# Kernel tuning notes

Hardware: AMD Instinct MI355X
Metric: run time of the kernel (lower is better)

The kernel has to match this reference:

```python
import jax, jax.numpy as jnp
import numpy as np
import math

B, C, N, M = 4, 128, 4096, 4096

def setup_inputs() -> dict:
    key = jax.random.key(0)
    ks = jax.random.split(key, 8)
    return {
        "x1": jax.random.normal(ks[0], (B, C, N), dtype=jnp.float32),
        "p1": jax.random.normal(ks[1], (B, 3, N), dtype=jnp.float32),
        "x2": jax.random.normal(ks[2], (B, C, M), dtype=jnp.float32),
        "p2": jax.random.normal(ks[3], (B, 3, M), dtype=jnp.float32),
        "Wq": jax.random.normal(ks[4], (C, C), dtype=jnp.float32) * 0.05,
        "Wk": jax.random.normal(ks[5], (C, C), dtype=jnp.float32) * 0.05,
        "Wv": jax.random.normal(ks[6], (C, C), dtype=jnp.float32) * 0.05,
        "Wpos": jax.random.normal(ks[7], (C, 3), dtype=jnp.float32) * 0.05,
    }

def reference(x1, p1, x2, p2, Wq, Wk, Wv, Wpos):
    # Conv1d with kernel_size=1, no bias == per-point matmul over channel dim.
    # NOTE: original forward uses self.pos for BOTH p1 and p2 (pos1 conv unused).
    pos = jnp.einsum('ck,bkn->bcn', Wpos, p1)   # [B,C,N]
    pos1 = jnp.einsum('ck,bkm->bcm', Wpos, p2)  # [B,C,M]
    q = jnp.einsum('dc,bcn->bdn', Wq, x1 + pos)   # [B,C,N]
    k = jnp.einsum('dc,bcm->bdm', Wk, x2 + pos1)  # [B,C,M]
    v = jnp.einsum('dc,bcm->bdm', Wv, x2)         # [B,C,M]
    scale = math.sqrt(q.shape[1])  # sqrt(C) -- q.shape[-2] in (B,C,N) layout
    energy = jnp.einsum('bcn,bcm->bnm', q, k) / scale  # [B,N,M]
    attention = jax.nn.softmax(energy, axis=-1)
    vout = jnp.einsum('bnm,bcm->bnc', attention, v)    # [B,N,C]
    out = jnp.swapaxes(vout, 1, 2) + x1                # [B,C,N] residual
    return jnp.swapaxes(out, 1, 2)                     # [B,N,C]
```

## Files before the change

### kernel.cpp

```cpp
#include <hip/hip_runtime.h>
#include <hip/hip_bf16.h>

#define B_ 4
#define C_ 128
#define N_ 4096
#define M_ 4096

typedef __bf16 bf16;
typedef __bf16 bf16x8 __attribute__((ext_vector_type(8)));
typedef float f32x4 __attribute__((ext_vector_type(4)));
typedef float f32x16 __attribute__((ext_vector_type(16)));

#define MFMA16(a, b, c) __builtin_amdgcn_mfma_f32_16x16x32_bf16(a, b, c, 0, 0, 0)
#define MFMA32(a, b, c) __builtin_amdgcn_mfma_f32_32x32x16_bf16(a, b, c, 0, 0, 0)

__device__ inline bf16x8 cvt8(const float* p8) {
    float4 a = *(const float4*)p8;
    float4 b = *(const float4*)(p8 + 4);
    bf16x8 r;
    r[0] = (bf16)a.x; r[1] = (bf16)a.y; r[2] = (bf16)a.z; r[3] = (bf16)a.w;
    r[4] = (bf16)b.x; r[5] = (bf16)b.y; r[6] = (bf16)b.z; r[7] = (bf16)b.w;
    return r;
}

__device__ inline void gll16(const bf16* g, bf16* l) {
    __builtin_amdgcn_global_load_lds(
        (const __attribute__((address_space(1))) void*)g,
        (__attribute__((address_space(3))) void*)l, 16, 0, 0);
}

__global__ __launch_bounds__(768) void proj_kernel(
    const float* __restrict__ x1, const float* __restrict__ p1,
    const float* __restrict__ x2, const float* __restrict__ p2,
    const float* __restrict__ Wq, const float* __restrict__ Wk,
    const float* __restrict__ Wv, const float* __restrict__ Wpos,
    bf16* __restrict__ Qt, bf16* __restrict__ Kt, bf16* __restrict__ Vt) {
    __shared__ __align__(16) bf16 xp1[64 * 136];
    __shared__ __align__(16) bf16 xp2[64 * 136];
    __shared__ __align__(16) bf16 xr2[64 * 136];
    __shared__ float pp1[3 * 64], pp2[3 * 64], wls[384];

    const int t = threadIdx.x;
    const int b = blockIdx.y;
    const int n0 = blockIdx.x * 64;

    if (t < 48) {
        int k3 = t / 16, i4 = (t & 15) * 4;
        *(float4*)&pp1[k3 * 64 + i4] = *(const float4*)(p1 + ((size_t)b * 3 + k3) * N_ + n0 + i4);
    } else if (t < 96) {
        int tt = t - 48;
        int k3 = tt / 16, i4 = (tt & 15) * 4;
        *(float4*)&pp2[k3 * 64 + i4] = *(const float4*)(p2 + ((size_t)b * 3 + k3) * N_ + n0 + i4);
    } else if (t < 192) {
        int i4 = (t - 96) * 4;
        *(float4*)&wls[i4] = *(const float4*)(Wpos + i4);
    }
    __syncthreads();

    for (int s = t; s < 2048; s += 768) {
        int c = s >> 4, n4 = (s & 15) * 4;
        float4 xv = *(const float4*)(x1 + ((size_t)b * C_ + c) * N_ + n0 + n4);
        float w0 = wls[c * 3 + 0], w1 = wls[c * 3 + 1], w2 = wls[c * 3 + 2];
        const float* xa = &xv.x;
        #pragma unroll
        for (int j = 0; j < 4; ++j) {
            float pos = w0 * pp1[n4 + j] + w1 * pp1[64 + n4 + j] + w2 * pp1[128 + n4 + j];
            xp1[(n4 + j) * 136 + c] = (bf16)(xa[j] + pos);
        }
    }
    for (int s = t; s < 2048; s += 768) {
        int c = s >> 4, n4 = (s & 15) * 4;
        float4 xv = *(const float4*)(x2 + ((size_t)b * C_ + c) * N_ + n0 + n4);
        float w0 = wls[c * 3 + 0], w1 = wls[c * 3 + 1], w2 = wls[c * 3 + 2];
        const float* xa = &xv.x;
        #pragma unroll
        for (int j = 0; j < 4; ++j) {
            float pos = w0 * pp2[n4 + j] + w1 * pp2[64 + n4 + j] + w2 * pp2[128 + n4 + j];
            xp2[(n4 + j) * 136 + c] = (bf16)(xa[j] + pos);
            xr2[(n4 + j) * 136 + c] = (bf16)xa[j];
        }
    }
    __syncthreads();

    const int w = t >> 6;
    const int lane = t & 63;
    const int col = lane & 15, quad = lane >> 4;
    const int role = w >> 2, band = w & 3;
    const int nl = band * 16 + col;
    const int n = n0 + nl;

    const bf16* src = (role == 0) ? xp1 : (role == 1) ? xp2 : xr2;
    const float* Wm = (role == 0) ? Wq : (role == 1) ? Wk : Wv;

    bf16x8 bx[4];
    #pragma unroll
    for (int cs = 0; cs < 4; ++cs)
        bx[cs] = *(const bf16x8*)&src[nl * 136 + cs * 32 + quad * 8];

    #pragma unroll
    for (int dt = 0; dt < 8; ++dt) {
        f32x4 acc = {0.f, 0.f, 0.f, 0.f};
        #pragma unroll
        for (int cs = 0; cs < 4; ++cs) {
            bf16x8 wf = cvt8(Wm + (dt * 16 + col) * 128 + cs * 32 + quad * 8);
            acc = MFMA16(wf, bx[cs], acc);
        }
        if (role < 2) {
            bf16* Ot = (role == 0) ? Qt : Kt;
            union { ushort4 u4; bf16 h[4]; } pk;
            #pragma unroll
            for (int r = 0; r < 4; ++r) pk.h[r] = (bf16)acc[r];
            *(ushort4*)(Ot + ((size_t)b * N_ + n) * C_ + dt * 16 + quad * 4) = pk.u4;
        } else {
            #pragma unroll
            for (int r = 0; r < 4; ++r)
                Vt[((size_t)b * C_ + dt * 16 + quad * 4 + r) * (size_t)M_ + n] = (bf16)acc[r];
        }
    }
}

__global__ __launch_bounds__(256, 2) void attn_kernel(
    const bf16* __restrict__ Qt, const bf16* __restrict__ Kt,
    const bf16* __restrict__ Vt, const float* __restrict__ x1,
    float* __restrict__ out) {
    __shared__ __align__(16) char smem[75776];
    bf16* kb = (bf16*)smem;
    bf16* vb = (bf16*)(smem + 32768);
    bf16* pb = (bf16*)(smem + 65536);

    const int t = threadIdx.x;
    const int w = t >> 6;
    const int lane = t & 63;
    const int col = lane & 31;
    const int hi = lane >> 5;

    const int g0 = blockIdx.x;
    const int xcd = g0 & 7;
    const int b = xcd >> 1;
    const int qt = (xcd & 1) + ((g0 >> 3) << 1);
    const int n0 = qt * 32;

    const float KS = 0.12752107168406815f;

    const bf16* Kbase = Kt + (size_t)b * M_ * C_;
    const bf16* Vbase = Vt + (size_t)b * C_ * M_;

    bf16x8 qf[8];
    {
        const bf16* Qb = Qt + ((size_t)b * N_ + n0 + col) * C_ + hi * 8;
        #pragma unroll
        for (int cs = 0; cs < 8; ++cs)
            qf[cs] = *(const bf16x8*)(Qb + cs * 16);
    }

    f32x16 oacc[4];
    #pragma unroll
    for (int i = 0; i < 4; ++i)
        #pragma unroll
        for (int j = 0; j < 16; ++j) oacc[i][j] = 0.f;
    float lacc[16];
    #pragma unroll
    for (int r = 0; r < 16; ++r) lacc[r] = 0.f;

    const int key_l = (w << 5) + col;
    const char* kbp = (const char*)kb + key_l * 256;
    const int kxor = (key_l & 7) << 4;
    bf16* pbw = pb + w * 1280;

    auto stageK = [&](int m0) {
        #pragma unroll
        for (int i = 0; i < 8; ++i) {
            int g = ((w << 3) + i) * 64 + lane;
            int key = g >> 4;
            int sp = (g & 15) ^ (key & 7);
            gll16(Kbase + (size_t)(m0 + key) * C_ + sp * 8, kb + ((w << 3) + i) * 512);
        }
    };
    auto stageV = [&](int m0) {
        #pragma unroll
        for (int i = 0; i < 8; ++i) {
            int g = ((w << 3) + i) * 64 + lane;
            int c = g >> 4;
            int sp = (g & 15) ^ (c & 7);
            gll16(Vbase + (size_t)c * M_ + m0 + sp * 8, vb + ((w << 3) + i) * 512);
        }
    };

    stageK(0);
    stageV(0);
    __syncthreads();

    for (int ch = 0; ch < 32; ++ch) {
        f32x16 sacc;
        #pragma unroll
        for (int j = 0; j < 16; ++j) sacc[j] = 0.f;
        __builtin_amdgcn_s_setprio(1);
        #pragma unroll
        for (int cs = 0; cs < 8; ++cs) {
            bf16x8 kf = *(const bf16x8*)(kbp + ((((cs << 1) + hi) << 4) ^ kxor));
            sacc = MFMA32(qf[cs], kf, sacc);
        }
        __builtin_amdgcn_s_setprio(0);

        __syncthreads();
        if (ch < 31) stageK((ch + 1) << 7);

        #pragma unroll
        for (int r = 0; r < 16; ++r) {
            float e = fminf(sacc[r] * KS, 60.f);
            float p = __builtin_amdgcn_exp2f(e);
            lacc[r] += p;
            int q = (r & 3) + ((r >> 2) << 3) + (hi << 2);
            pbw[q * 40 + col] = (bf16)p;
        }
        asm volatile("s_waitcnt lgkmcnt(0)" ::: "memory");

        bf16x8 af0 = *(const bf16x8*)&pbw[col * 40 + hi * 8];
        bf16x8 af1 = *(const bf16x8*)&pbw[col * 40 + 16 + hi * 8];

        __builtin_amdgcn_s_setprio(1);
        #pragma unroll
        for (int ct = 0; ct < 4; ++ct) {
            int c = (ct << 5) + col;
            const char* vbp = (const char*)vb + c * 256;
            int vxor = (c & 7) << 4;
            bf16x8 vf0 = *(const bf16x8*)(vbp + ((((w << 2) + hi) << 4) ^ vxor));
            bf16x8 vf1 = *(const bf16x8*)(vbp + ((((w << 2) + 2 + hi) << 4) ^ vxor));
            oacc[ct] = MFMA32(af0, vf0, oacc[ct]);
            oacc[ct] = MFMA32(af1, vf1, oacc[ct]);
        }
        __builtin_amdgcn_s_setprio(0);

        __syncthreads();
        if (ch < 31) stageV((ch + 1) << 7);
    }

    __syncthreads();

    float* obuf = (float*)smem;
    float* lps  = (float*)(smem + 67584);

    #pragma unroll
    for (int r = 0; r < 16; ++r)
        #pragma unroll
        for (int off = 1; off < 32; off <<= 1)
            lacc[r] += __shfl_xor(lacc[r], off, 64);

    if (col == 0) {
        #pragma unroll
        for (int r = 0; r < 16; ++r) {
            int q = (r & 3) + ((r >> 2) << 3) + (hi << 2);
            lps[(w << 5) + q] = lacc[r];
        }
    }
    #pragma unroll
    for (int ct = 0; ct < 4; ++ct)
        #pragma unroll
        for (int r = 0; r < 16; ++r) {
            int q = (r & 3) + ((r >> 2) << 3) + (hi << 2);
            obuf[w * 4224 + q * 132 + (ct << 5) + col] = oacc[ct][r];
        }
    __syncthreads();

    const int c2 = lane << 1;
    #pragma unroll
    for (int j = 0; j < 8; ++j) {
        int q = (w << 3) + j;
        float s0 = 0.f, s1 = 0.f;
        #pragma unroll
        for (int p = 0; p < 4; ++p) {
            s0 += obuf[p * 4224 + q * 132 + c2];
            s1 += obuf[p * 4224 + q * 132 + c2 + 1];
        }
        float lsum = lps[q] + lps[32 + q] + lps[64 + q] + lps[96 + q];
        float linv = 1.0f / lsum;
        int n = n0 + q;
        float o0 = s0 * linv + x1[((size_t)b * C_ + c2) * N_ + n];
        float o1 = s1 * linv + x1[((size_t)b * C_ + c2 + 1) * N_ + n];
        *(float2*)&out[((size_t)b * N_ + n) * C_ + c2] = make_float2(o0, o1);
    }
}

extern "C" void kernel_launch(void* const* d_in, const int* in_sizes, int n_in,
                              void* d_out, int out_size, void* d_ws, size_t ws_size,
                              hipStream_t stream) {
    const float* x1   = (const float*)d_in[0];
    const float* p1   = (const float*)d_in[1];
    const float* x2   = (const float*)d_in[2];
    const float* p2   = (const float*)d_in[3];
    const float* Wq   = (const float*)d_in[4];
    const float* Wk   = (const float*)d_in[5];
    const float* Wv   = (const float*)d_in[6];
    const float* Wpos = (const float*)d_in[7];
    float* out = (float*)d_out;

    bf16* Qt = (bf16*)d_ws;
    bf16* Kt = Qt + (size_t)B_ * N_ * C_;
    bf16* Vt = Kt + (size_t)B_ * M_ * C_;

    proj_kernel<<<dim3(64, B_), dim3(768), 0, stream>>>(
        x1, p1, x2, p2, Wq, Wk, Wv, Wpos, Qt, Kt, Vt);
    attn_kernel<<<dim3(512), dim3(256), 0, stream>>>(Qt, Kt, Vt, x1, out);
}
```

Measured before the change: 169.1 us.

## Transpose S MFMA to keep P in registers and loosen attention barriers

The attention kernel now computes S^T (K as the A operand) and splits it across two accumulators. It builds the P operand in registers with packed bf16 conversion and a cross-half lane shuffle, which removes the LDS round trip for P and the per-row shuffle reductions. The __syncthreads calls become vmcnt-based waits plus raw s_barrier so the next K/V tile loads overlap compute, and the LDS swizzle is widened to 16. The weights are also pre-converted to bf16 by a new small kernel that writes into the output buffer as scratch. This trades an extra launch and more fragile hand-written synchronization for less LDS traffic and fewer stalls.

```diff
diff --git a/kernel.cpp b/kernel.cpp
--- a/kernel.cpp
+++ b/kernel.cpp
@@ -14,26 +14,35 @@
 #define MFMA16(a, b, c) __builtin_amdgcn_mfma_f32_16x16x32_bf16(a, b, c, 0, 0, 0)
 #define MFMA32(a, b, c) __builtin_amdgcn_mfma_f32_32x32x16_bf16(a, b, c, 0, 0, 0)
 
-__device__ inline bf16x8 cvt8(const float* p8) {
-    float4 a = *(const float4*)p8;
-    float4 b = *(const float4*)(p8 + 4);
-    bf16x8 r;
-    r[0] = (bf16)a.x; r[1] = (bf16)a.y; r[2] = (bf16)a.z; r[3] = (bf16)a.w;
-    r[4] = (bf16)b.x; r[5] = (bf16)b.y; r[6] = (bf16)b.z; r[7] = (bf16)b.w;
-    return r;
-}
-
 __device__ inline void gll16(const bf16* g, bf16* l) {
     __builtin_amdgcn_global_load_lds(
         (const __attribute__((address_space(1))) void*)g,
         (__attribute__((address_space(3))) void*)l, 16, 0, 0);
 }
 
+__device__ inline unsigned cvtpk(float a, float b) {
+    unsigned r;
+    asm("v_cvt_pk_bf16_f32 %0, %1, %2" : "=v"(r) : "v"(a), "v"(b));
+    return r;
+}
+
+__global__ __launch_bounds__(256) void wcvt_kernel(
+    const float* __restrict__ Wq, const float* __restrict__ Wk,
+    const float* __restrict__ Wv, bf16* __restrict__ Wb) {
+    int i = (blockIdx.x * 256 + threadIdx.x) * 4;
+    const float* src = (i < 16384) ? Wq : (i < 32768) ? Wk : Wv;
+    int off = i & 16383;
+    float4 v = *(const float4*)(src + off);
+    union { ushort4 u4; bf16 h[4]; } pk;
+    pk.h[0] = (bf16)v.x; pk.h[1] = (bf16)v.y;
+    pk.h[2] = (bf16)v.z; pk.h[3] = (bf16)v.w;
+    *(ushort4*)(Wb + i) = pk.u4;
+}
+
 __global__ __launch_bounds__(768) void proj_kernel(
     const float* __restrict__ x1, const float* __restrict__ p1,
     const float* __restrict__ x2, const float* __restrict__ p2,
-    const float* __restrict__ Wq, const float* __restrict__ Wk,
-    const float* __restrict__ Wv, const float* __restrict__ Wpos,
+    const bf16* __restrict__ Wb, const float* __restrict__ Wpos,
     bf16* __restrict__ Qt, bf16* __restrict__ Kt, bf16* __restrict__ Vt) {
     __shared__ __align__(16) bf16 xp1[64 * 136];
     __shared__ __align__(16) bf16 xp2[64 * 136];
@@ -90,7 +99,7 @@
     const int n = n0 + nl;
 
     const bf16* src = (role == 0) ? xp1 : (role == 1) ? xp2 : xr2;
-    const float* Wm = (role == 0) ? Wq : (role == 1) ? Wk : Wv;
+    const bf16* Wm = Wb + role * 16384;
 
     bf16x8 bx[4];
     #pragma unroll
@@ -102,7 +111,7 @@
         f32x4 acc = {0.f, 0.f, 0.f, 0.f};
         #pragma unroll
         for (int cs = 0; cs < 4; ++cs) {
-            bf16x8 wf = cvt8(Wm + (dt * 16 + col) * 128 + cs * 32 + quad * 8);
+            bf16x8 wf = *(const bf16x8*)(Wm + (dt * 16 + col) * 128 + cs * 32 + quad * 8);
             acc = MFMA16(wf, bx[cs], acc);
         }
         if (role < 2) {
@@ -123,10 +132,9 @@
     const bf16* __restrict__ Qt, const bf16* __restrict__ Kt,
     const bf16* __restrict__ Vt, const float* __restrict__ x1,
     float* __restrict__ out) {
-    __shared__ __align__(16) char smem[75776];
+    __shared__ __align__(16) char smem[66048];
     bf16* kb = (bf16*)smem;
     bf16* vb = (bf16*)(smem + 32768);
-    bf16* pb = (bf16*)(smem + 65536);
 
     const int t = threadIdx.x;
     const int w = t >> 6;
@@ -158,21 +166,18 @@
     for (int i = 0; i < 4; ++i)
         #pragma unroll
         for (int j = 0; j < 16; ++j) oacc[i][j] = 0.f;
-    float lacc[16];
-    #pragma unroll
-    for (int r = 0; r < 16; ++r) lacc[r] = 0.f;
+    float lacc = 0.f;
 
     const int key_l = (w << 5) + col;
     const char* kbp = (const char*)kb + key_l * 256;
-    const int kxor = (key_l & 7) << 4;
-    bf16* pbw = pb + w * 1280;
+    const int kxor = (key_l & 15) << 4;
 
     auto stageK = [&](int m0) {
         #pragma unroll
         for (int i = 0; i < 8; ++i) {
             int g = ((w << 3) + i) * 64 + lane;
             int key = g >> 4;
-            int sp = (g & 15) ^ (key & 7);
+            int sp = (g & 15) ^ (key & 15);
             gll16(Kbase + (size_t)(m0 + key) * C_ + sp * 8, kb + ((w << 3) + i) * 512);
         }
     };
@@ -181,49 +186,80 @@
         for (int i = 0; i < 8; ++i) {
             int g = ((w << 3) + i) * 64 + lane;
             int c = g >> 4;
-            int sp = (g & 15) ^ (c & 7);
+            int sp = (g & 15) ^ (c & 15);
             gll16(Vbase + (size_t)c * M_ + m0 + sp * 8, vb + ((w << 3) + i) * 512);
         }
     };
 
     stageK(0);
     stageV(0);
-    __syncthreads();
 
     for (int ch = 0; ch < 32; ++ch) {
-        f32x16 sacc;
-        #pragma unroll
-        for (int j = 0; j < 16; ++j) sacc[j] = 0.f;
+        asm volatile("s_waitcnt vmcnt(8)" ::: "memory");
+        __builtin_amdgcn_sched_barrier(0);
+
+        f32x16 s0a, s1a;
+        #pragma unroll
+        for (int j = 0; j < 16; ++j) { s0a[j] = 0.f; s1a[j] = 0.f; }
         __builtin_amdgcn_s_setprio(1);
         #pragma unroll
-        for (int cs = 0; cs < 8; ++cs) {
+        for (int cs = 0; cs < 4; ++cs) {
             bf16x8 kf = *(const bf16x8*)(kbp + ((((cs << 1) + hi) << 4) ^ kxor));
-            sacc = MFMA32(qf[cs], kf, sacc);
+            s0a = MFMA32(kf, qf[cs], s0a);
+        }
+        #pragma unroll
+        for (int cs = 4; cs < 8; ++cs) {
+            bf16x8 kf = *(const bf16x8*)(kbp + ((((cs << 1) + hi) << 4) ^ kxor));
+            s1a = MFMA32(kf, qf[cs], s1a);
         }
         __builtin_amdgcn_s_setprio(0);
 
-        __syncthreads();
-        if (ch < 31) stageK((ch + 1) << 7);
-
+        if (ch < 31) {
+            asm volatile("s_waitcnt lgkmcnt(0)" ::: "memory");
+            __builtin_amdgcn_sched_barrier(0);
+            stageK((ch + 1) << 7);
+        }
+
+        float p[16];
         #pragma unroll
         for (int r = 0; r < 16; ++r) {
-            float e = fminf(sacc[r] * KS, 60.f);
-            float p = __builtin_amdgcn_exp2f(e);
-            lacc[r] += p;
-            int q = (r & 3) + ((r >> 2) << 3) + (hi << 2);
-            pbw[q * 40 + col] = (bf16)p;
-        }
-        asm volatile("s_waitcnt lgkmcnt(0)" ::: "memory");
-
-        bf16x8 af0 = *(const bf16x8*)&pbw[col * 40 + hi * 8];
-        bf16x8 af1 = *(const bf16x8*)&pbw[col * 40 + 16 + hi * 8];
+            float e = fminf((s0a[r] + s1a[r]) * KS, 60.f);
+            p[r] = __builtin_amdgcn_exp2f(e);
+        }
+        {
+            float s01 = (p[0] + p[1]) + (p[2] + p[3]);
+            float s23 = (p[4] + p[5]) + (p[6] + p[7]);
+            float s45 = (p[8] + p[9]) + (p[10] + p[11]);
+            float s67 = (p[12] + p[13]) + (p[14] + p[15]);
+            lacc += (s01 + s23) + (s45 + s67);
+        }
+        unsigned W0 = cvtpk(p[0], p[1]),  W1 = cvtpk(p[2], p[3]);
+        unsigned W2 = cvtpk(p[4], p[5]),  W3 = cvtpk(p[6], p[7]);
+        unsigned W4 = cvtpk(p[8], p[9]),  W5 = cvtpk(p[10], p[11]);
+        unsigned W6 = cvtpk(p[12], p[13]), W7 = cvtpk(p[14], p[15]);
+        unsigned X0 = hi ? W0 : W2, X1 = hi ? W1 : W3;
+        unsigned Y0 = hi ? W4 : W6, Y1 = hi ? W5 : W7;
+        X0 = __shfl_xor(X0, 32, 64);  X1 = __shfl_xor(X1, 32, 64);
+        Y0 = __shfl_xor(Y0, 32, 64);  Y1 = __shfl_xor(Y1, 32, 64);
+        uint4 u0, u1;
+        u0.x = hi ? X0 : W0;  u0.y = hi ? X1 : W1;
+        u0.z = hi ? W2 : X0;  u0.w = hi ? W3 : X1;
+        u1.x = hi ? Y0 : W4;  u1.y = hi ? Y1 : W5;
+        u1.z = hi ? W6 : Y0;  u1.w = hi ? W7 : Y1;
+        bf16x8 af0 = __builtin_bit_cast(bf16x8, u0);
+        bf16x8 af1 = __builtin_bit_cast(bf16x8, u1);
+
+        if (ch < 31) asm volatile("s_waitcnt vmcnt(8)" ::: "memory");
+        else         asm volatile("s_waitcnt vmcnt(0)" ::: "memory");
+        __builtin_amdgcn_sched_barrier(0);
+        __builtin_amdgcn_s_barrier();
 
         __builtin_amdgcn_s_setprio(1);
         #pragma unroll
         for (int ct = 0; ct < 4; ++ct) {
             int c = (ct << 5) + col;
             const char* vbp = (const char*)vb + c * 256;
-            int vxor = (c & 7) << 4;
+            int vxor = (c & 15) << 4;
             bf16x8 vf0 = *(const bf16x8*)(vbp + ((((w << 2) + hi) << 4) ^ vxor));
             bf16x8 vf1 = *(const bf16x8*)(vbp + ((((w << 2) + 2 + hi) << 4) ^ vxor));
             oacc[ct] = MFMA32(af0, vf0, oacc[ct]);
@@ -231,34 +267,26 @@
         }
         __builtin_amdgcn_s_setprio(0);
 
-        __syncthreads();
+        asm volatile("s_waitcnt lgkmcnt(0)" ::: "memory");
+        __builtin_amdgcn_sched_barrier(0);
+        __builtin_amdgcn_s_barrier();
         if (ch < 31) stageV((ch + 1) << 7);
     }
 
-    __syncthreads();
+    __builtin_amdgcn_s_barrier();
 
     float* obuf = (float*)smem;
-    float* lps  = (float*)(smem + 67584);
-
-    #pragma unroll
-    for (int r = 0; r < 16; ++r)
-        #pragma unroll
-        for (int off = 1; off < 32; off <<= 1)
-            lacc[r] += __shfl_xor(lacc[r], off, 64);
-
-    if (col == 0) {
+    float* lps  = (float*)(smem + 65536);
+
+    lacc += __shfl_xor(lacc, 32, 64);
+    if (hi == 0) lps[(w << 5) + col] = lacc;
+
+    #pragma unroll
+    for (int ct = 0; ct < 4; ++ct)
         #pragma unroll
         for (int r = 0; r < 16; ++r) {
             int q = (r & 3) + ((r >> 2) << 3) + (hi << 2);
-            lps[(w << 5) + q] = lacc[r];
-        }
-    }
-    #pragma unroll
-    for (int ct = 0; ct < 4; ++ct)
-        #pragma unroll
-        for (int r = 0; r < 16; ++r) {
-            int q = (r & 3) + ((r >> 2) << 3) + (hi << 2);
-            obuf[w * 4224 + q * 132 + (ct << 5) + col] = oacc[ct][r];
+            obuf[w * 4096 + q * 128 + (ct << 5) + col] = oacc[ct][r];
         }
     __syncthreads();
 
@@ -268,9 +296,9 @@
         int q = (w << 3) + j;
         float s0 = 0.f, s1 = 0.f;
         #pragma unroll
-        for (int p = 0; p < 4; ++p) {
-            s0 += obuf[p * 4224 + q * 132 + c2];
-            s1 += obuf[p * 4224 + q * 132 + c2 + 1];
+        for (int pp = 0; pp < 4; ++pp) {
+            float2 v = *(const float2*)&obuf[pp * 4096 + q * 128 + c2];
+            s0 += v.x; s1 += v.y;
         }
         float lsum = lps[q] + lps[32 + q] + lps[64 + q] + lps[96 + q];
         float linv = 1.0f / lsum;
@@ -298,7 +326,10 @@
     bf16* Kt = Qt + (size_t)B_ * N_ * C_;
     bf16* Vt = Kt + (size_t)B_ * M_ * C_;
 
+    bf16* Wb = (bf16*)d_out;
+
+    wcvt_kernel<<<dim3(48), dim3(256), 0, stream>>>(Wq, Wk, Wv, Wb);
     proj_kernel<<<dim3(64, B_), dim3(768), 0, stream>>>(
-        x1, p1, x2, p2, Wq, Wk, Wv, Wpos, Qt, Kt, Vt);
+        x1, p1, x2, p2, Wb, Wpos, Qt, Kt, Vt);
     attn_kernel<<<dim3(512), dim3(256), 0, stream>>>(Qt, Kt, Vt, x1, out);
 }
```

New measurement: 152.8 us. 1.11x faster.
